# Performance work log

Hardware: AMD Instinct MI355X
Metric: run time of the kernel (lower is better)

Reference implementation:

```python
import jax, jax.numpy as jnp
import numpy as np

B, N, SK, D, H = 4, 1024, 1024, 1024, 16
HD = D // H  # head_dim = 64


def _ln(x, w, b):
    # torch LayerNorm: biased variance, eps=1e-6
    m = x.mean(-1, keepdims=True)
    v = x.var(-1, keepdims=True)
    return (x - m) * jax.lax.rsqrt(v + 1e-6) * w + b


def setup_inputs() -> dict:
    key = jax.random.key(0)
    ks = jax.random.split(key, 16)
    def w(k, shape, s=0.02):
        return jax.random.normal(k, shape, jnp.float32) * s
    return dict(
        x=jax.random.normal(ks[0], (B, N, D), jnp.float32),
        k=jax.random.normal(ks[1], (N, H, SK, HD), jnp.float32),
        v=jax.random.normal(ks[2], (N, H, SK, HD), jnp.float32),
        qkv_w=w(ks[3], (D, 3 * D)), qkv_b=w(ks[4], (3 * D,)),
        sa_proj_w=w(ks[5], (D, D)), sa_proj_b=w(ks[6], (D,)),
        q_w=w(ks[7], (D, D)), q_b=w(ks[8], (D,)),
        ed_proj_w=w(ks[9], (D, D)), ed_proj_b=w(ks[10], (D,)),
        fc1_w=w(ks[11], (D, 4 * D)), fc1_b=w(ks[12], (4 * D,)),
        fc2_w=w(ks[13], (4 * D, D)), fc2_b=w(ks[14], (D,)),
        ln1_w=jnp.ones((D,)), ln1_b=jnp.zeros((D,)),
        ln2_w=jnp.ones((D,)), ln2_b=jnp.zeros((D,)),
        ln3_w=jnp.ones((D,)), ln3_b=jnp.zeros((D,)),
    )


def reference(x, k, v, qkv_w, qkv_b, sa_proj_w, sa_proj_b, q_w, q_b,
              ed_proj_w, ed_proj_b, fc1_w, fc1_b, fc2_w, fc2_b,
              ln1_w, ln1_b, ln2_w, ln2_b, ln3_w, ln3_b):
    scale = HD ** -0.5
    # ---- SelfAttention (faithful to the original, unusual einsums) ----
    qkv = (x @ qkv_w + qkv_b).reshape(B, N, 3, H, HD).transpose(2, 1, 3, 0, 4)
    q_s, k_s, v_s = qkv[0], qkv[1], qkv[2]  # each [N, H, B, HD]
    # no shared contraction index between k and q -> outer product of reductions
    dp = jnp.einsum('kabc,qdef->qabe', k_s, q_s) * scale  # [N, H, B, B]
    sc = jax.nn.softmax(dp, axis=-1)  # attn_p = 0.0 -> dropout is identity
    wa = jnp.einsum('qabc,kdef->bqaf', sc, v_s).reshape(B, N, D)
    sa = wa @ sa_proj_w + sa_proj_b
    h1 = _ln(sa + x, ln1_w, ln1_b)
    # ---- EncoderDecoderAttention ----
    qc = (h1 @ q_w + q_b).reshape(B, N, H, HD).transpose(1, 2, 0, 3)  # [N, H, B, HD]
    dp2 = jnp.einsum('abkd,abqd->abqk', k, qc) * scale  # [N, H, B, SK]
    sc2 = jax.nn.softmax(dp2, axis=-1)
    wa2 = jnp.einsum('abts,abse->tabe', sc2, v).reshape(B, N, D)
    ca = wa2 @ ed_proj_w + ed_proj_b
    h2 = _ln(ca + x, ln2_w, ln2_b)  # residual uses x (as in source)
    # ---- MLP (exact GELU, p=0 dropout) ----
    z = jax.nn.gelu(h2 @ fc1_w + fc1_b, approximate=False) @ fc2_w + fc2_b
    return _ln(z + h2, ln3_w, ln3_b)
```

## Files before the change

### kernel.cpp

```cpp
#include <hip/hip_runtime.h>
#include <hip/hip_bf16.h>
#include <math.h>

typedef __attribute__((ext_vector_type(8))) short bf16x8;
typedef __attribute__((ext_vector_type(4))) float f32x4;

__device__ __forceinline__ void gll16(const void* g, const void* l) {
  __builtin_amdgcn_global_load_lds((__attribute__((address_space(1))) void*)g,
                                   (__attribute__((address_space(3))) void*)l, 16, 0, 0);
}

__global__ __launch_bounds__(256) void k_transpose_bf16(
    const float* __restrict__ W, __hip_bfloat16* __restrict__ WT, int R, int C)
{
  __shared__ float t[32][33];
  const int c0 = blockIdx.x << 5, r0 = blockIdx.y << 5;
  const int tx = threadIdx.x & 31, ty = threadIdx.x >> 5;
#pragma unroll
  for (int i = 0; i < 32; i += 8)
    t[ty + i][tx] = W[(size_t)(r0 + ty + i) * C + c0 + tx];
  __syncthreads();
#pragma unroll
  for (int i = 0; i < 32; i += 8)
    WT[(size_t)(c0 + ty + i) * R + r0 + tx] = __float2bfloat16(t[tx][ty + i]);
}

__global__ __launch_bounds__(256) void k_colsum_part(const float* __restrict__ x, float* __restrict__ part) {
  const int d = blockIdx.x * 256 + threadIdx.x;
  const int r0 = blockIdx.y * 128;
  float acc = 0.f;
  for (int r = 0; r < 128; ++r) acc += x[(size_t)(r0 + r) * 1024 + d];
  part[blockIdx.y * 1024 + d] = acc;
}
__global__ __launch_bounds__(256) void k_colsum_fin(const float* __restrict__ part, float* __restrict__ Xsum) {
  const int d = blockIdx.x * 256 + threadIdx.x;
  float acc = 0.f;
  for (int y = 0; y < 32; ++y) acc += part[y * 1024 + d];
  Xsum[d] = acc;
}

__global__ __launch_bounds__(256) void k_matvec_t(const float* __restrict__ Xsum,
                                                  const float* __restrict__ qkv_w,
                                                  float* __restrict__ tmpt) {
  __shared__ float red[8][32];
  const int j = blockIdx.x * 32 + (threadIdx.x & 31);
  const int rg = threadIdx.x >> 5;
  float acc = 0.f;
  for (int r = rg; r < 1024; r += 8)
    acc += Xsum[r] * qkv_w[(size_t)r * 3072 + 2048 + j];
  red[rg][threadIdx.x & 31] = acc;
  __syncthreads();
  if (threadIdx.x < 32) {
    float s = 0.f;
    for (int gq = 0; gq < 8; ++gq) s += red[gq][threadIdx.x];
    tmpt[blockIdx.x * 32 + threadIdx.x] = s;
  }
}

__global__ void k_vsum(const float* __restrict__ tmpt, const float* __restrict__ qkv_b,
                       float* __restrict__ Vsum) {
  const int f = threadIdx.x;
  float acc = 0.f;
  for (int h = 0; h < 16; ++h)
    acc += tmpt[h * 64 + f] + 4096.0f * qkv_b[2048 + h * 64 + f];
  Vsum[f] = acc;
}

__global__ __launch_bounds__(256) void k_matvec_sa(const float* __restrict__ Vsum,
                                                   const float* __restrict__ saw,
                                                   const float* __restrict__ sab,
                                                   float* __restrict__ sarow) {
  __shared__ float red[8][32];
  const int j = blockIdx.x * 32 + (threadIdx.x & 31);
  const int rg = threadIdx.x >> 5;
  float acc = 0.f;
  for (int r = rg; r < 1024; r += 8)
    acc += Vsum[r & 63] * saw[(size_t)r * 1024 + j];
  red[rg][threadIdx.x & 31] = acc;
  __syncthreads();
  if (threadIdx.x < 32) {
    float s = 0.f;
    for (int gq = 0; gq < 8; ++gq) s += red[gq][threadIdx.x];
    sarow[blockIdx.x * 32 + threadIdx.x] = s + sab[blockIdx.x * 32 + threadIdx.x];
  }
}

__global__ __launch_bounds__(256) void k_ln(
    const float* __restrict__ a, const float* __restrict__ b,
    const float* __restrict__ rowadd, const float* __restrict__ w,
    const float* __restrict__ bias, float* __restrict__ outF,
    __hip_bfloat16* __restrict__ outB)
{
  const size_t base = (size_t)blockIdx.x * 1024;
  float v[4];
  float s1 = 0.f, s2 = 0.f;
#pragma unroll
  for (int i = 0; i < 4; ++i) {
    const int d = threadIdx.x + (i << 8);
    float t = a[base + d];
    if (b) t += b[base + d];
    if (rowadd) t += rowadd[d];
    v[i] = t; s1 += t; s2 += t * t;
  }
#pragma unroll
  for (int o = 32; o; o >>= 1) { s1 += __shfl_xor(s1, o); s2 += __shfl_xor(s2, o); }
  __shared__ float r1[4], r2[4];
  const int wv = threadIdx.x >> 6;
  if ((threadIdx.x & 63) == 0) { r1[wv] = s1; r2[wv] = s2; }
  __syncthreads();
  s1 = r1[0] + r1[1] + r1[2] + r1[3];
  s2 = r2[0] + r2[1] + r2[2] + r2[3];
  const float mean = s1 * (1.0f / 1024.0f);
  const float var = s2 * (1.0f / 1024.0f) - mean * mean;
  const float inv = rsqrtf(var + 1e-6f);
#pragma unroll
  for (int i = 0; i < 4; ++i) {
    const int d = threadIdx.x + (i << 8);
    const float y = (v[i] - mean) * inv * w[d] + bias[d];
    if (outF) outF[base + d] = y;
    if (outB) outB[base + d] = __float2bfloat16(y);
  }
}

template<int GELU, int OUTBF>
__global__ __launch_bounds__(256) void k_gemm_bt(
    const __hip_bfloat16* __restrict__ A, const __hip_bfloat16* __restrict__ BT,
    const float* __restrict__ bias, float* __restrict__ outF,
    __hip_bfloat16* __restrict__ outB, int M, int N, int K)
{
  __shared__ __align__(16) __hip_bfloat16 As[128 * 32];
  __shared__ __align__(16) __hip_bfloat16 Bs[128 * 32];
  const int tid = threadIdx.x;
  const int wave = tid >> 6, lane = tid & 63;
  const int m0 = blockIdx.y << 7, n0 = blockIdx.x << 7;
  const int wr = wave >> 1, wc = wave & 1;
  const int fr = lane & 15, fq = lane >> 4;
  f32x4 acc[4][4] = {};
  const int srow = (lane >> 2);
  const int scol = (lane & 3) * 8;
  for (int k0 = 0; k0 < K; k0 += 32) {
#pragma unroll
    for (int i = 0; i < 2; ++i) {
      const int chunk = wave * 2 + i;
      const int row = (chunk << 4) + srow;
      gll16(A + (size_t)(m0 + row) * K + k0 + scol, As + (chunk << 9));
      gll16(BT + (size_t)(n0 + row) * K + k0 + scol, Bs + (chunk << 9));
    }
    __syncthreads();
    bf16x8 af[4], bfr[4];
#pragma unroll
    for (int m = 0; m < 4; ++m)
      af[m] = *(const bf16x8*)(As + ((wr << 6) + (m << 4) + fr) * 32 + (fq << 3));
#pragma unroll
    for (int nn = 0; nn < 4; ++nn)
      bfr[nn] = *(const bf16x8*)(Bs + ((wc << 6) + (nn << 4) + fr) * 32 + (fq << 3));
#pragma unroll
    for (int m = 0; m < 4; ++m)
#pragma unroll
      for (int nn = 0; nn < 4; ++nn)
        acc[m][nn] = __builtin_amdgcn_mfma_f32_16x16x32_bf16(af[m], bfr[nn], acc[m][nn], 0, 0, 0);
    __syncthreads();
  }
#pragma unroll
  for (int m = 0; m < 4; ++m) {
#pragma unroll
    for (int nn = 0; nn < 4; ++nn) {
      const int col = n0 + (wc << 6) + (nn << 4) + fr;
      const float bv = bias[col];
#pragma unroll
      for (int j = 0; j < 4; ++j) {
        const int row = m0 + (wr << 6) + (m << 4) + (fq << 2) + j;
        float vv = acc[m][nn][j] + bv;
        if (GELU) vv = 0.5f * vv * (1.0f + erff(vv * 0.70710678118654752f));
        if (OUTBF) outB[(size_t)row * N + col] = __float2bfloat16(vv);
        else       outF[(size_t)row * N + col] = vv;
      }
    }
  }
}

__global__ __launch_bounds__(256) void k_attn(
    const float* __restrict__ kk, const float* __restrict__ vvg,
    const float* __restrict__ qc, __hip_bfloat16* __restrict__ wa2b)
{
  __shared__ __align__(16) float tile[128 * 64];
  __shared__ float p[4 * 1024];
  __shared__ __align__(16) float ql[4 * 64];
  __shared__ float denom[4];
  const int tid = threadIdx.x;
  const int wave = tid >> 6, lane = tid & 63;
  const int n = blockIdx.x >> 4, h = blockIdx.x & 15;
  const size_t kvbase = (size_t)(n * 16 + h) * (1024 * 64);
  {
    const int b = tid >> 6, d = tid & 63;
    ql[tid] = qc[((size_t)b * 1024 + n) * 1024 + h * 64 + d] * 0.125f;
  }
  __syncthreads();
  const int s_l = tid & 127;
  const int q0 = (tid >> 7) * 2;
  const int sx = s_l & 15;
  for (int t8 = 0; t8 < 8; ++t8) {
    const int s0 = t8 << 7;
#pragma unroll
    for (int i = 0; i < 8; ++i) {
      const int chunk = (wave << 3) + i;
      const int rl = (chunk << 2) + (lane >> 4);
      const int slot = (lane & 15) ^ (rl & 15);
      gll16(kk + kvbase + (size_t)(s0 + rl) * 64 + (slot << 2), tile + (chunk << 8));
    }
    __syncthreads();
    float a0 = 0.f, a1 = 0.f;
    const float4* qv0 = (const float4*)(ql + q0 * 64);
    const float4* qv1 = (const float4*)(ql + q0 * 64 + 64);
#pragma unroll
    for (int d4 = 0; d4 < 16; ++d4) {
      const float4 kv = *(const float4*)(tile + s_l * 64 + ((d4 ^ sx) << 2));
      const float4 qa = qv0[d4];
      const float4 qb = qv1[d4];
      a0 += kv.x * qa.x + kv.y * qa.y + kv.z * qa.z + kv.w * qa.w;
      a1 += kv.x * qb.x + kv.y * qb.y + kv.z * qb.z + kv.w * qb.w;
    }
    p[q0 * 1024 + s0 + s_l] = a0;
    p[(q0 + 1) * 1024 + s0 + s_l] = a1;
    __syncthreads();
  }
  {
    const int q = wave;
    float mx = -1e30f;
#pragma unroll
    for (int j = 0; j < 16; ++j) mx = fmaxf(mx, p[q * 1024 + (j << 6) + lane]);
#pragma unroll
    for (int o = 32; o; o >>= 1) mx = fmaxf(mx, __shfl_xor(mx, o));
    float sum = 0.f;
#pragma unroll
    for (int j = 0; j < 16; ++j) {
      const float e = __expf(p[q * 1024 + (j << 6) + lane] - mx);
      p[q * 1024 + (j << 6) + lane] = e;
      sum += e;
    }
#pragma unroll
    for (int o = 32; o; o >>= 1) sum += __shfl_xor(sum, o);
    if (lane == 0) denom[q] = sum;
  }
  __syncthreads();
  const int e = lane;
  const int qq = wave;
  const int eslotbase = (e >> 2);
  const int ebyte = (e & 3);
  float acc = 0.f;
  for (int t8 = 0; t8 < 8; ++t8) {
    const int s0 = t8 << 7;
#pragma unroll
    for (int i = 0; i < 8; ++i) {
      const int chunk = (wave << 3) + i;
      const int rl = (chunk << 2) + (lane >> 4);
      const int slot = (lane & 15) ^ (rl & 15);
      gll16(vvg + kvbase + (size_t)(s0 + rl) * 64 + (slot << 2), tile + (chunk << 8));
    }
    __syncthreads();
    const float* prow = p + qq * 1024 + s0;
    for (int s = 0; s < 128; s += 4) {
      const float4 pv4 = *(const float4*)(prow + s);
      acc += pv4.x * tile[(s    ) * 64 + ((eslotbase ^ ((s    ) & 15)) << 2) + ebyte];
      acc += pv4.y * tile[(s + 1) * 64 + ((eslotbase ^ ((s + 1) & 15)) << 2) + ebyte];
      acc += pv4.z * tile[(s + 2) * 64 + ((eslotbase ^ ((s + 2) & 15)) << 2) + ebyte];
      acc += pv4.w * tile[(s + 3) * 64 + ((eslotbase ^ ((s + 3) & 15)) << 2) + ebyte];
    }
    __syncthreads();
  }
  const float o = acc / denom[qq];
  wa2b[((size_t)qq * 1024 + n) * 1024 + h * 64 + e] = __float2bfloat16(o);
}

extern "C" void kernel_launch(void* const* d_in, const int* in_sizes, int n_in,
                              void* d_out, int out_size, void* d_ws, size_t ws_size,
                              hipStream_t stream)
{
  (void)in_sizes; (void)n_in; (void)out_size; (void)ws_size;
  const float* x     = (const float*)d_in[0];
  const float* kin   = (const float*)d_in[1];
  const float* vin   = (const float*)d_in[2];
  const float* qkv_w = (const float*)d_in[3];
  const float* qkv_b = (const float*)d_in[4];
  const float* sa_w  = (const float*)d_in[5];
  const float* sa_b  = (const float*)d_in[6];
  const float* q_w   = (const float*)d_in[7];
  const float* q_b   = (const float*)d_in[8];
  const float* ed_w  = (const float*)d_in[9];
  const float* ed_b  = (const float*)d_in[10];
  const float* fc1_w = (const float*)d_in[11];
  const float* fc1_b = (const float*)d_in[12];
  const float* fc2_w = (const float*)d_in[13];
  const float* fc2_b = (const float*)d_in[14];
  const float* ln1_w = (const float*)d_in[15];
  const float* ln1_b = (const float*)d_in[16];
  const float* ln2_w = (const float*)d_in[17];
  const float* ln2_b = (const float*)d_in[18];
  const float* ln3_w = (const float*)d_in[19];
  const float* ln3_b = (const float*)d_in[20];
  float* out = (float*)d_out;

  char* ws = (char*)d_ws;
  constexpr size_t MB = 1024ull * 1024ull;
  float* part  = (float*)(ws + 0);
  float* Xsum  = (float*)(ws + 128 * 1024);
  float* tmpt  = (float*)(ws + 128 * 1024 + 4096);
  float* Vsum  = (float*)(ws + 128 * 1024 + 8192);
  float* sarow = (float*)(ws + 128 * 1024 + 12288);
  float*          qc   = (float*)(ws + 1 * MB);
  __hip_bfloat16* h1b  = (__hip_bfloat16*)(ws + 17 * MB);
  float*          ca   = (float*)(ws + 25 * MB);
  float*          h2   = (float*)(ws + 41 * MB);
  __hip_bfloat16* h2b  = (__hip_bfloat16*)(ws + 57 * MB);
  __hip_bfloat16* g    = (__hip_bfloat16*)(ws + 65 * MB);
  __hip_bfloat16* qwT  = (__hip_bfloat16*)(ws + 97 * MB);
  __hip_bfloat16* edwT = (__hip_bfloat16*)(ws + 99 * MB);
  __hip_bfloat16* f1wT = (__hip_bfloat16*)(ws + 101 * MB);
  __hip_bfloat16* f2wT = (__hip_bfloat16*)(ws + 109 * MB);
  float* z = qc;
  __hip_bfloat16* wa2b = h1b;

  k_transpose_bf16<<<dim3(32, 32), 256, 0, stream>>>(q_w, qwT, 1024, 1024);
  k_transpose_bf16<<<dim3(32, 32), 256, 0, stream>>>(ed_w, edwT, 1024, 1024);
  k_transpose_bf16<<<dim3(128, 32), 256, 0, stream>>>(fc1_w, f1wT, 1024, 4096);
  k_transpose_bf16<<<dim3(32, 128), 256, 0, stream>>>(fc2_w, f2wT, 4096, 1024);
  k_colsum_part<<<dim3(4, 32), 256, 0, stream>>>(x, part);
  k_colsum_fin<<<dim3(4), 256, 0, stream>>>(part, Xsum);
  k_matvec_t<<<dim3(32), 256, 0, stream>>>(Xsum, qkv_w, tmpt);
  k_vsum<<<dim3(1), 64, 0, stream>>>(tmpt, qkv_b, Vsum);
  k_matvec_sa<<<dim3(32), 256, 0, stream>>>(Vsum, sa_w, sa_b, sarow);
  k_ln<<<dim3(4096), 256, 0, stream>>>(x, nullptr, sarow, ln1_w, ln1_b, nullptr, h1b);
  k_gemm_bt<0, 0><<<dim3(8, 32), 256, 0, stream>>>(h1b, qwT, q_b, qc, nullptr, 4096, 1024, 1024);
  k_attn<<<dim3(16384), 256, 0, stream>>>(kin, vin, qc, wa2b);
  k_gemm_bt<0, 0><<<dim3(8, 32), 256, 0, stream>>>(wa2b, edwT, ed_b, ca, nullptr, 4096, 1024, 1024);
  k_ln<<<dim3(4096), 256, 0, stream>>>(ca, x, nullptr, ln2_w, ln2_b, h2, h2b);
  k_gemm_bt<1, 1><<<dim3(32, 32), 256, 0, stream>>>(h2b, f1wT, fc1_b, nullptr, g, 4096, 4096, 1024);
  k_gemm_bt<0, 0><<<dim3(8, 32), 256, 0, stream>>>(g, f2wT, fc2_b, z, nullptr, 4096, 1024, 4096);
  k_ln<<<dim3(4096), 256, 0, stream>>>(z, h2, nullptr, ln3_w, ln3_b, out, nullptr);
}
```

Measured before the change: 1.839 ms.

## Double-buffer K/V tiles in cross-attention and vectorize LayerNorm and PV accumulation

The cross-attention kernel now stages 64-row K/V tiles into two LDS buffers, issuing the load for the next tile before computing on the current one. This overlaps global-to-LDS transfers with the dot products and needs one barrier per tile instead of two, and the first V tile is prefetched during the last K step. The PV stage switches to float4 LDS reads with a cross-lane shuffle reduction and packed bf16 stores, and q is held in registers. LayerNorm is rewritten to use float4 loads and stores. In exchange, register pressure rises from the 16 float4 q values held per thread.

```diff
diff --git a/kernel.cpp b/kernel.cpp
--- a/kernel.cpp
+++ b/kernel.cpp
@@ -8,6 +8,11 @@
 __device__ __forceinline__ void gll16(const void* g, const void* l) {
   __builtin_amdgcn_global_load_lds((__attribute__((address_space(1))) void*)g,
                                    (__attribute__((address_space(3))) void*)l, 16, 0, 0);
+}
+
+__device__ __forceinline__ unsigned short bf16bits(float f) {
+  __hip_bfloat16 h = __float2bfloat16(f);
+  return *reinterpret_cast<unsigned short*>(&h);
 }
 
 __global__ __launch_bounds__(256) void k_transpose_bf16(
@@ -92,16 +97,14 @@
     __hip_bfloat16* __restrict__ outB)
 {
   const size_t base = (size_t)blockIdx.x * 1024;
-  float v[4];
-  float s1 = 0.f, s2 = 0.f;
-#pragma unroll
-  for (int i = 0; i < 4; ++i) {
-    const int d = threadIdx.x + (i << 8);
-    float t = a[base + d];
-    if (b) t += b[base + d];
-    if (rowadd) t += rowadd[d];
-    v[i] = t; s1 += t; s2 += t * t;
-  }
+  const int d4 = threadIdx.x << 2;
+  float4 t = *(const float4*)(a + base + d4);
+  if (b) { const float4 u = *(const float4*)(b + base + d4);
+           t.x += u.x; t.y += u.y; t.z += u.z; t.w += u.w; }
+  if (rowadd) { const float4 u = *(const float4*)(rowadd + d4);
+                t.x += u.x; t.y += u.y; t.z += u.z; t.w += u.w; }
+  float s1 = t.x + t.y + t.z + t.w;
+  float s2 = t.x * t.x + t.y * t.y + t.z * t.z + t.w * t.w;
 #pragma unroll
   for (int o = 32; o; o >>= 1) { s1 += __shfl_xor(s1, o); s2 += __shfl_xor(s2, o); }
   __shared__ float r1[4], r2[4];
@@ -113,12 +116,16 @@
   const float mean = s1 * (1.0f / 1024.0f);
   const float var = s2 * (1.0f / 1024.0f) - mean * mean;
   const float inv = rsqrtf(var + 1e-6f);
-#pragma unroll
-  for (int i = 0; i < 4; ++i) {
-    const int d = threadIdx.x + (i << 8);
-    const float y = (v[i] - mean) * inv * w[d] + bias[d];
-    if (outF) outF[base + d] = y;
-    if (outB) outB[base + d] = __float2bfloat16(y);
+  const float4 w4 = *(const float4*)(w + d4);
+  const float4 b4 = *(const float4*)(bias + d4);
+  const float y0 = (t.x - mean) * inv * w4.x + b4.x;
+  const float y1 = (t.y - mean) * inv * w4.y + b4.y;
+  const float y2 = (t.z - mean) * inv * w4.z + b4.z;
+  const float y3 = (t.w - mean) * inv * w4.w + b4.w;
+  if (outF) *(float4*)(outF + base + d4) = make_float4(y0, y1, y2, y3);
+  if (outB) {
+    ushort4 u4; u4.x = bf16bits(y0); u4.y = bf16bits(y1); u4.z = bf16bits(y2); u4.w = bf16bits(y3);
+    *(ushort4*)(outB + base + d4) = u4;
   }
 }
 
@@ -183,7 +190,7 @@
     const float* __restrict__ kk, const float* __restrict__ vvg,
     const float* __restrict__ qc, __hip_bfloat16* __restrict__ wa2b)
 {
-  __shared__ __align__(16) float tile[128 * 64];
+  __shared__ __align__(16) float tile[2][64 * 64];
   __shared__ float p[4 * 1024];
   __shared__ __align__(16) float ql[4 * 64];
   __shared__ float denom[4];
@@ -191,85 +198,88 @@
   const int wave = tid >> 6, lane = tid & 63;
   const int n = blockIdx.x >> 4, h = blockIdx.x & 15;
   const size_t kvbase = (size_t)(n * 16 + h) * (1024 * 64);
-  {
-    const int b = tid >> 6, d = tid & 63;
-    ql[tid] = qc[((size_t)b * 1024 + n) * 1024 + h * 64 + d] * 0.125f;
-  }
-  __syncthreads();
-  const int s_l = tid & 127;
-  const int q0 = (tid >> 7) * 2;
-  const int sx = s_l & 15;
-  for (int t8 = 0; t8 < 8; ++t8) {
-    const int s0 = t8 << 7;
-#pragma unroll
-    for (int i = 0; i < 8; ++i) {
-      const int chunk = (wave << 3) + i;
+
+  ql[tid] = qc[((size_t)wave * 1024 + n) * 1024 + h * 64 + lane] * 0.125f;
+
+  auto STAGE = [&](const float* __restrict__ src, int bi, int s0) {
+#pragma unroll
+    for (int i = 0; i < 4; ++i) {
+      const int chunk = (wave << 2) + i;
       const int rl = (chunk << 2) + (lane >> 4);
       const int slot = (lane & 15) ^ (rl & 15);
-      gll16(kk + kvbase + (size_t)(s0 + rl) * 64 + (slot << 2), tile + (chunk << 8));
-    }
+      gll16(src + kvbase + (size_t)(s0 + rl) * 64 + (slot << 2), tile[bi] + (chunk << 8));
+    }
+  };
+
+  STAGE(kk, 0, 0);
+  __syncthreads();
+
+  float4 qv[16];
+#pragma unroll
+  for (int i = 0; i < 16; ++i) qv[i] = *(const float4*)(ql + wave * 64 + (i << 2));
+
+  const int sx = lane & 15;
+  for (int t = 0; t < 16; ++t) {
+    if (t < 15) STAGE(kk, (t + 1) & 1, (t + 1) << 6);
+    else        STAGE(vvg, 0, 0);
+    const float* tl = tile[t & 1];
+    float a0 = 0.f;
+#pragma unroll
+    for (int d4 = 0; d4 < 16; ++d4) {
+      const float4 kv = *(const float4*)(tl + lane * 64 + ((d4 ^ sx) << 2));
+      const float4 qa = qv[d4];
+      a0 += kv.x * qa.x + kv.y * qa.y + kv.z * qa.z + kv.w * qa.w;
+    }
+    p[wave * 1024 + (t << 6) + lane] = a0;
     __syncthreads();
-    float a0 = 0.f, a1 = 0.f;
-    const float4* qv0 = (const float4*)(ql + q0 * 64);
-    const float4* qv1 = (const float4*)(ql + q0 * 64 + 64);
-#pragma unroll
-    for (int d4 = 0; d4 < 16; ++d4) {
-      const float4 kv = *(const float4*)(tile + s_l * 64 + ((d4 ^ sx) << 2));
-      const float4 qa = qv0[d4];
-      const float4 qb = qv1[d4];
-      a0 += kv.x * qa.x + kv.y * qa.y + kv.z * qa.z + kv.w * qa.w;
-      a1 += kv.x * qb.x + kv.y * qb.y + kv.z * qb.z + kv.w * qb.w;
-    }
-    p[q0 * 1024 + s0 + s_l] = a0;
-    p[(q0 + 1) * 1024 + s0 + s_l] = a1;
-    __syncthreads();
-  }
+  }
+
   {
-    const int q = wave;
     float mx = -1e30f;
 #pragma unroll
-    for (int j = 0; j < 16; ++j) mx = fmaxf(mx, p[q * 1024 + (j << 6) + lane]);
+    for (int j = 0; j < 16; ++j) mx = fmaxf(mx, p[wave * 1024 + (j << 6) + lane]);
 #pragma unroll
     for (int o = 32; o; o >>= 1) mx = fmaxf(mx, __shfl_xor(mx, o));
     float sum = 0.f;
 #pragma unroll
     for (int j = 0; j < 16; ++j) {
-      const float e = __expf(p[q * 1024 + (j << 6) + lane] - mx);
-      p[q * 1024 + (j << 6) + lane] = e;
+      const float e = __expf(p[wave * 1024 + (j << 6) + lane] - mx);
+      p[wave * 1024 + (j << 6) + lane] = e;
       sum += e;
     }
 #pragma unroll
     for (int o = 32; o; o >>= 1) sum += __shfl_xor(sum, o);
-    if (lane == 0) denom[q] = sum;
-  }
-  __syncthreads();
-  const int e = lane;
-  const int qq = wave;
-  const int eslotbase = (e >> 2);
-  const int ebyte = (e & 3);
-  float acc = 0.f;
-  for (int t8 = 0; t8 < 8; ++t8) {
-    const int s0 = t8 << 7;
-#pragma unroll
-    for (int i = 0; i < 8; ++i) {
-      const int chunk = (wave << 3) + i;
-      const int rl = (chunk << 2) + (lane >> 4);
-      const int slot = (lane & 15) ^ (rl & 15);
-      gll16(vvg + kvbase + (size_t)(s0 + rl) * 64 + (slot << 2), tile + (chunk << 8));
+    if (lane == 0) denom[wave] = sum;
+  }
+  __syncthreads();
+
+  const int sg = lane >> 4, e4 = lane & 15;
+  float4 acc4 = make_float4(0.f, 0.f, 0.f, 0.f);
+  for (int t = 0; t < 16; ++t) {
+    if (t < 15) STAGE(vvg, (t + 1) & 1, (t + 1) << 6);
+    const float* tl = tile[t & 1];
+    const float* prow = p + wave * 1024 + (t << 6);
+#pragma unroll
+    for (int so = 0; so < 16; ++so) {
+      const int s = (so << 2) + sg;
+      const float pw = prow[s];
+      const float4 vv = *(const float4*)(tl + s * 64 + ((e4 ^ (s & 15)) << 2));
+      acc4.x += pw * vv.x; acc4.y += pw * vv.y; acc4.z += pw * vv.z; acc4.w += pw * vv.w;
     }
     __syncthreads();
-    const float* prow = p + qq * 1024 + s0;
-    for (int s = 0; s < 128; s += 4) {
-      const float4 pv4 = *(const float4*)(prow + s);
-      acc += pv4.x * tile[(s    ) * 64 + ((eslotbase ^ ((s    ) & 15)) << 2) + ebyte];
-      acc += pv4.y * tile[(s + 1) * 64 + ((eslotbase ^ ((s + 1) & 15)) << 2) + ebyte];
-      acc += pv4.z * tile[(s + 2) * 64 + ((eslotbase ^ ((s + 2) & 15)) << 2) + ebyte];
-      acc += pv4.w * tile[(s + 3) * 64 + ((eslotbase ^ ((s + 3) & 15)) << 2) + ebyte];
-    }
-    __syncthreads();
-  }
-  const float o = acc / denom[qq];
-  wa2b[((size_t)qq * 1024 + n) * 1024 + h * 64 + e] = __float2bfloat16(o);
+  }
+#pragma unroll
+  for (int o = 16; o <= 32; o <<= 1) {
+    acc4.x += __shfl_xor(acc4.x, o); acc4.y += __shfl_xor(acc4.y, o);
+    acc4.z += __shfl_xor(acc4.z, o); acc4.w += __shfl_xor(acc4.w, o);
+  }
+  if (sg == 0) {
+    const float inv = 1.0f / denom[wave];
+    ushort4 u4;
+    u4.x = bf16bits(acc4.x * inv); u4.y = bf16bits(acc4.y * inv);
+    u4.z = bf16bits(acc4.z * inv); u4.w = bf16bits(acc4.w * inv);
+    *(ushort4*)(wa2b + ((size_t)wave * 1024 + n) * 1024 + h * 64 + (e4 << 2)) = u4;
+  }
 }
 
 extern "C" void kernel_launch(void* const* d_in, const int* in_sizes, int n_in,
```

After: 1.830 ms. Within noise of the previous version (-0.5%).
